# Kernel tuning notes

Hardware: AMD Instinct MI355X
Metric: run time of the kernel (lower is better)

Reference implementation:

```python
import jax, jax.numpy as jnp
import numpy as np

N, E, B = 524288, 4194304, 16384
F_IN, FP, TV, GOUT = 14, 1024, 256, 32
EPS = 1e-5
SLOPE = 0.2  # PyG GATConv default negative_slope


def setup_inputs() -> dict:
    key = jax.random.key(0)
    ks = iter(jax.random.split(key, 64))
    def nrm(shape, scale=1.0):
        return jax.random.normal(next(ks), shape, dtype=jnp.float32) * scale
    def uni(shape, lo, hi):
        return jax.random.uniform(next(ks), shape, dtype=jnp.float32, minval=lo, maxval=hi)
    def bn(d):  # [gamma, beta, running_mean, running_var]
        return jnp.stack([uni((d,), 0.5, 1.5), nrm((d,), 0.1), nrm((d,), 0.1), uni((d,), 0.5, 1.5)])
    return {
        'x': nrm((N, F_IN)),
        'edge_index': jax.random.randint(next(ks), (2, E), 0, N, dtype=jnp.int32),
        'batch': jnp.sort(jax.random.randint(next(ks), (N,), 0, B, dtype=jnp.int32)),
        'fingerprint': nrm((B, FP)),
        'transformer_features': nrm((B, TV)),
        'W1': nrm((F_IN, F_IN), 0.3), 'a_src1': nrm((F_IN,), 0.3), 'a_dst1': nrm((F_IN,), 0.3), 'b1': nrm((F_IN,), 0.1),
        'W2': nrm((F_IN, GOUT), 0.3), 'a_src2': nrm((GOUT,), 0.3), 'a_dst2': nrm((GOUT,), 0.3), 'b2': nrm((GOUT,), 0.1),
        'fc1_w': nrm((FP, 400), 0.04), 'fc1_b': nrm((400,), 0.1), 'bn1': bn(400),
        'fc2_w': nrm((400, 200), 0.07), 'fc2_b': nrm((200,), 0.1), 'bn2': bn(200),
        'fc3_w': nrm((TV, 400), 0.08), 'fc3_b': nrm((400,), 0.1), 'bn3': bn(400),
        'fc4_w': nrm((400, 200), 0.07), 'fc4_b': nrm((200,), 0.1), 'bn4': bn(200),
        'fcc1_w': nrm((GOUT + 400, 100), 0.07), 'fcc1_b': nrm((100,), 0.1), 'bnc': bn(100),
        'fcc2_w': nrm((100, 1), 0.1), 'fcc2_b': nrm((1,), 0.1),
    }


def _bn(h, p):  # eval-mode BatchNorm1d with packed params [4, d]
    return (h - p[2]) * jax.lax.rsqrt(p[3] + EPS) * p[0] + p[1]


def _gat(x, W, a_s, a_d, b, src, dst, n):
    # PyG GATConv, heads=1: messages flow src -> dst, softmax over incoming edges per dst
    h = x @ W                                   # [n, C]
    e = jax.nn.leaky_relu((h @ a_s)[src] + (h @ a_d)[dst], SLOPE)  # [E_tot]
    m = jax.lax.stop_gradient(jax.ops.segment_max(e, dst, num_segments=n))
    w = jnp.exp(e - m[dst])
    denom = jax.ops.segment_sum(w, dst, num_segments=n)
    alpha = w / denom[dst]
    out = jax.ops.segment_sum(alpha[:, None] * h[src], dst, num_segments=n)
    return out + b


def reference(x, edge_index, batch, fingerprint, transformer_features,
              W1, a_src1, a_dst1, b1, W2, a_src2, a_dst2, b2,
              fc1_w, fc1_b, bn1, fc2_w, fc2_b, bn2,
              fc3_w, fc3_b, bn3, fc4_w, fc4_b, bn4,
              fcc1_w, fcc1_b, bnc, fcc2_w, fcc2_b):
    n = x.shape[0]
    loop = jnp.arange(n, dtype=edge_index.dtype)  # add_self_loops
    src = jnp.concatenate([edge_index[0], loop])
    dst = jnp.concatenate([edge_index[1], loop])
    g = jax.nn.relu(_gat(x, W1, a_src1, a_dst1, b1, src, dst, n))
    g = jax.nn.relu(_gat(g, W2, a_src2, a_dst2, b2, src, dst, n))
    pool = jax.ops.segment_sum(g, batch, num_segments=B)  # global_add_pool -> [B, GOUT]
    fp = jax.nn.relu(_bn(fingerprint @ fc1_w + fc1_b, bn1))
    fp = jax.nn.relu(_bn(fp @ fc2_w + fc2_b, bn2))
    tv = jax.nn.relu(_bn(transformer_features @ fc3_w + fc3_b, bn3))
    tv = jax.nn.relu(_bn(tv @ fc4_w + fc4_b, bn4))
    comb = jnp.concatenate([pool, fp, tv], axis=1)  # [B, 32+200+200]
    comb = jax.nn.relu(_bn(comb @ fcc1_w + fcc1_b, bnc))
    return comb @ fcc2_w + fcc2_b  # [B, 1]
```

## Files before the change

### kernel.cpp

```cpp
#include <hip/hip_runtime.h>

typedef unsigned short u16;
typedef unsigned int u32;
typedef __attribute__((ext_vector_type(8))) short bf16x8;
typedef __attribute__((ext_vector_type(4))) float f32x4;

#define N_NODES 524288
#define N_EDGES 4194304
#define N_GRAPH 16384
#define P_BLOCKS 1024
#define BKTS 512
#define DPB 1024
#define CAP 8960

__device__ __forceinline__ float bf2f(u16 u){ u32 x=((u32)u)<<16; float f; __builtin_memcpy(&f,&x,4); return f; }
__device__ __forceinline__ float lo2f(u32 u){ u32 x=u<<16; float f; __builtin_memcpy(&f,&x,4); return f; }
__device__ __forceinline__ float hi2f(u32 u){ u32 x=u&0xffff0000u; float f; __builtin_memcpy(&f,&x,4); return f; }
__device__ __forceinline__ u16 f2bf(float f){ u32 x; __builtin_memcpy(&x,&f,4); return (u16)((x + 0x7fffu + ((x>>16)&1u))>>16); }
__device__ __forceinline__ float lrelu(float e){ return e>0.f? e : 0.2f*e; }
__device__ __forceinline__ float gload(const void* p, int i, int is32){
    return is32 ? ((const float*)p)[i] : bf2f(((const u16*)p)[i]);
}
__device__ __forceinline__ u32 fmax_key(float f){ u32 u; __builtin_memcpy(&u,&f,4); return (u>>31)? ~u : (u|0x80000000u); }
__device__ __forceinline__ float key_fmax(u32 k){ u32 u = (k>>31)? (k^0x80000000u) : ~k; float f; __builtin_memcpy(&f,&u,4); return f; }

__global__ __launch_bounds__(256) void k_detect(const u32* __restrict__ x, int* __restrict__ flag){
    __shared__ int cnt;
    if (threadIdx.x==0) cnt = 0;
    __syncthreads();
    int c = 0;
    for (int i = threadIdx.x; i < 1024; i += 256){
        u32 e = (x[i] >> 7) & 0xFF;
        if (e >= 110 && e <= 140) c++;
    }
    atomicAdd(&cnt, c);
    __syncthreads();
    if (threadIdx.x==0) *flag = (cnt < 512) ? 1 : 0;
}

__global__ __launch_bounds__(256) void k_p1(const int* __restrict__ dst, u32* __restrict__ tbl_bm){
    __shared__ u32 lh[BKTS];
    int t = threadIdx.x, blk = blockIdx.x;
    lh[t] = 0; lh[t+256] = 0;
    __syncthreads();
    int base = blk*4096;
    #pragma unroll
    for (int k=0;k<16;k++){
        int d = __builtin_nontemporal_load(dst + base + k*256 + t) & (N_NODES-1);
        atomicAdd(&lh[d>>10], 1);
    }
    __syncthreads();
    tbl_bm[blk*BKTS + t]       = lh[t];
    tbl_bm[blk*BKTS + t + 256] = lh[t+256];
}

__global__ __launch_bounds__(256) void k_ttbl(const u32* __restrict__ bm, u32* __restrict__ km){
    __shared__ u32 tile[32][33];
    int bx = blockIdx.x;
    int by = blockIdx.y;
    int tx = threadIdx.x & 31, ty = threadIdx.x >> 5;
    #pragma unroll
    for (int r=0;r<32;r+=8)
        tile[ty+r][tx] = bm[(bx*32 + ty + r)*BKTS + by*32 + tx];
    __syncthreads();
    #pragma unroll
    for (int r=0;r<32;r+=8)
        km[(by*32 + ty + r)*P_BLOCKS + bx*32 + tx] = tile[tx][ty+r];
}

__global__ __launch_bounds__(256) void k_scan1(int* __restrict__ data, int* __restrict__ bsums){
    __shared__ int sh[256];
    int b = blockIdx.x, t = threadIdx.x;
    int base = b*1024 + t*4;
    int4 v = *(const int4*)(data + base);
    int s = v.x+v.y+v.z+v.w;
    sh[t] = s; __syncthreads();
    for (int off=1; off<256; off<<=1){
        int xv = (t>=off)? sh[t-off] : 0; __syncthreads();
        sh[t] += xv; __syncthreads();
    }
    int excl = sh[t] - s;
    if (t==255) bsums[b] = sh[255];
    int4 o; o.x = excl; o.y = excl+v.x; o.z = o.y+v.y; o.w = o.z+v.z;
    *(int4*)(data + base) = o;
}

__global__ __launch_bounds__(256) void k_scan2(int* __restrict__ bsums){
    __shared__ int sh[256];
    int t = threadIdx.x;
    int v0 = bsums[2*t], v1 = bsums[2*t+1];
    int s = v0+v1; sh[t] = s; __syncthreads();
    for (int off=1; off<256; off<<=1){
        int xv = (t>=off)? sh[t-off] : 0; __syncthreads();
        sh[t] += xv; __syncthreads();
    }
    int excl = sh[t] - s;
    bsums[2*t] = excl; bsums[2*t+1] = excl + v0;
}

__global__ __launch_bounds__(256) void k_scan3(int* __restrict__ scan, const int* __restrict__ bsums, int N_, int E_){
    int i = blockIdx.x*256 + threadIdx.x;
    if (i < N_) scan[i] += bsums[i>>10];
    if (i == 0) scan[N_] = E_;
}

__global__ __launch_bounds__(256) void k_p2(const int* __restrict__ src, const int* __restrict__ dst,
        const u32* __restrict__ km, u32* __restrict__ btab){
    __shared__ u32 lh[BKTS], lofs[BKTS], gofs[BKTS];
    __shared__ u32 stage[4096], tgt[4096];
    __shared__ u32 red[256];
    int t = threadIdx.x, blk = blockIdx.x;
    lh[t] = 0; lh[t+256] = 0;
    __syncthreads();
    u32 pr[16], rk[16]; u16 bk[16];
    int base = blk*4096;
    #pragma unroll
    for (int k=0;k<16;k++){
        int e = base + k*256 + t;
        int d = __builtin_nontemporal_load(dst+e) & (N_NODES-1);
        int s = __builtin_nontemporal_load(src+e) & (N_NODES-1);
        u32 b = (u32)d >> 10;
        bk[k] = (u16)b;
        pr[k] = (u32)(d & 1023) | ((u32)s << 10);
        rk[k] = atomicAdd(&lh[b], 1);
    }
    gofs[t]       = km[(size_t)t*P_BLOCKS + blk];
    gofs[t+256]   = km[(size_t)(t+256)*P_BLOCKS + blk];
    __syncthreads();
    u32 v0 = lh[2*t], v1 = lh[2*t+1];
    u32 s2 = v0+v1; red[t] = s2; __syncthreads();
    for (int off=1; off<256; off<<=1){
        u32 xv = (t>=off)? red[t-off] : 0; __syncthreads();
        red[t] += xv; __syncthreads();
    }
    u32 excl = red[t] - s2;
    lofs[2*t] = excl; lofs[2*t+1] = excl + v0;
    __syncthreads();
    #pragma unroll
    for (int k=0;k<16;k++){
        u32 p = lofs[bk[k]] + rk[k];
        stage[p] = pr[k];
        tgt[p]   = gofs[bk[k]] + rk[k];
    }
    __syncthreads();
    #pragma unroll
    for (int k=0;k<16;k++){
        int j = k*256 + t;
        btab[tgt[j]] = stage[j];
    }
}

__global__ __launch_bounds__(256) void k_p3(const u32* __restrict__ km, const u32* __restrict__ btab,
        int* __restrict__ rowptr, int* __restrict__ ssrc){
    __shared__ u32 fh[DPB], fo[DPB];
    __shared__ u32 red[256];
    __shared__ int sst[CAP];
    int t = threadIdx.x, b = blockIdx.x;
    u32 basep = km[(size_t)b*P_BLOCKS];
    u32 endp  = km[(size_t)(b+1)*P_BLOCKS];
    int cnt = (int)(endp - basep);
    #pragma unroll
    for (int i=t;i<DPB;i+=256) fh[i] = 0;
    __syncthreads();
    for (int j=t; j<cnt; j+=256){
        u32 p = btab[basep + j];
        atomicAdd(&fh[p & 1023], 1);
    }
    __syncthreads();
    u32 v0=fh[4*t], v1=fh[4*t+1], v2=fh[4*t+2], v3=fh[4*t+3];
    u32 s4 = v0+v1+v2+v3; red[t] = s4; __syncthreads();
    for (int off=1; off<256; off<<=1){
        u32 xv = (t>=off)? red[t-off] : 0; __syncthreads();
        red[t] += xv; __syncthreads();
    }
    u32 excl = red[t] - s4;
    fo[4*t]=excl; fo[4*t+1]=excl+v0; fo[4*t+2]=excl+v0+v1; fo[4*t+3]=excl+v0+v1+v2;
    __syncthreads();
    #pragma unroll
    for (int i=t;i<DPB;i+=256) rowptr[b*DPB + i] = (int)(basep + fo[i]);
    if (b == BKTS-1 && t == 0) rowptr[N_NODES] = (int)endp;
    __syncthreads();
    for (int j=t; j<cnt; j+=256){
        u32 p = btab[basep + j];
        u32 pos = atomicAdd(&fo[p & 1023], 1);
        if (pos < (u32)CAP) sst[pos] = (int)(p >> 10);
    }
    __syncthreads();
    for (int j=t; j<cnt; j+=256) ssrc[basep + j] = sst[j];
}

__global__ __launch_bounds__(256) void k_linear1(const void* __restrict__ x,
        const void* __restrict__ W1, const void* __restrict__ asw, const void* __restrict__ adw,
        u16* __restrict__ h1, float* __restrict__ ad1, u32* __restrict__ gkey,
        const int* __restrict__ flag){
    int is32 = *flag;
    __shared__ float Wf[196], av[14], dv[14];
    __shared__ float red[256];
    int t = threadIdx.x;
    if (t < 196) Wf[t] = gload(W1, t, is32);
    else if (t < 210) av[t-196] = gload(asw, t-196, is32);
    else if (t < 224) dv[t-210] = gload(adw, t-210, is32);
    __syncthreads();
    int i = blockIdx.x*256 + t;
    float xv[14];
    if (is32){
        const float* xr = (const float*)x + (size_t)i*14;
        #pragma unroll
        for (int k=0;k<14;k++) xv[k] = xr[k];
    } else {
        const u32* xr = (const u32*)((const u16*)x + (size_t)i*14);
        #pragma unroll
        for (int p=0;p<7;p++){ u32 u = xr[p]; xv[2*p]=lo2f(u); xv[2*p+1]=hi2f(u); }
    }
    float h[14];
    #pragma unroll
    for (int j=0;j<14;j++){ float s=0.f;
        #pragma unroll
        for (int k=0;k<14;k++) s += xv[k]*Wf[k*14+j];
        h[j]=s; }
    float a=0.f, d=0.f;
    #pragma unroll
    for (int j=0;j<14;j++){ a += h[j]*av[j]; d += h[j]*dv[j]; }
    ad1[i]=d;
    u32 ou[8];
    #pragma unroll
    for (int p=0;p<7;p++) ou[p] = (u32)f2bf(h[2*p]) | ((u32)f2bf(h[2*p+1])<<16);
    __builtin_memcpy(&ou[7], &a, 4);
    uint4* hp = (uint4*)(h1 + (size_t)i*16);
    hp[0] = make_uint4(ou[0],ou[1],ou[2],ou[3]);
    hp[1] = make_uint4(ou[4],ou[5],ou[6],ou[7]);
    red[t] = a; __syncthreads();
    for (int o=128;o;o>>=1){ if (t<o) red[t]=fmaxf(red[t],red[t+o]); __syncthreads(); }
    if (t==0) atomicMax(gkey, fmax_key(red[0]));
}

__global__ __launch_bounds__(256) void k_linear2(const u16* __restrict__ g1,
        const void* __restrict__ W2, const void* __restrict__ asw, const void* __restrict__ adw,
        u16* __restrict__ h2, float* __restrict__ as2, float* __restrict__ ad2,
        u32* __restrict__ gkey, const int* __restrict__ flag){
    int is32 = *flag;
    __shared__ float Wf[448], av[32], dv[32];
    __shared__ float red[256];
    int t = threadIdx.x;
    for (int idx=t; idx<448; idx+=256) Wf[idx] = gload(W2, idx, is32);
    if (t < 32) { av[t] = gload(asw, t, is32); dv[t] = gload(adw, t, is32); }
    __syncthreads();
    int i = blockIdx.x*256 + t;
    const uint4* gp = (const uint4*)(g1 + (size_t)i*16);
    uint4 q0 = gp[0], q1 = gp[1];
    u32 u[8] = {q0.x,q0.y,q0.z,q0.w,q1.x,q1.y,q1.z,q1.w};
    float gv[14];
    #pragma unroll
    for (int k=0;k<14;k++){ u32 uu=u[k>>1]; gv[k] = (k&1)? hi2f(uu) : lo2f(uu); }
    float h[32];
    #pragma unroll
    for (int j=0;j<32;j++) h[j]=0.f;
    #pragma unroll
    for (int k=0;k<14;k++){ float g_ = gv[k];
        #pragma unroll
        for (int j=0;j<32;j++) h[j] += g_*Wf[k*32+j]; }
    float a=0.f, d=0.f;
    #pragma unroll
    for (int j=0;j<32;j++){ a += h[j]*av[j]; d += h[j]*dv[j]; }
    as2[i]=a; ad2[i]=d;
    u32 ou[16];
    #pragma unroll
    for (int p=0;p<16;p++) ou[p] = (u32)f2bf(h[2*p]) | ((u32)f2bf(h[2*p+1])<<16);
    uint4* hp = (uint4*)(h2 + (size_t)i*32);
    hp[0]=make_uint4(ou[0],ou[1],ou[2],ou[3]);
    hp[1]=make_uint4(ou[4],ou[5],ou[6],ou[7]);
    hp[2]=make_uint4(ou[8],ou[9],ou[10],ou[11]);
    hp[3]=make_uint4(ou[12],ou[13],ou[14],ou[15]);
    red[t] = a; __syncthreads();
    for (int o=128;o;o>>=1){ if (t<o) red[t]=fmaxf(red[t],red[t+o]); __syncthreads(); }
    if (t==0) atomicMax(gkey, fmax_key(red[0]));
}

__global__ __launch_bounds__(256) void k_gather1(const int* __restrict__ rowptr, const int* __restrict__ ssrc,
        const u16* __restrict__ h1, const float* __restrict__ ad1, const u32* __restrict__ gkey,
        const void* __restrict__ b1, u16* __restrict__ g1, const int* __restrict__ flag){
    int is32 = *flag;
    int i = blockIdx.x*256 + threadIdx.x;
    float adv = ad1[i];
    float M = lrelu(key_fmax(*gkey) + adv);
    int beg = rowptr[i], end = rowptr[i+1];
    float acc[14], den;
    {
        const uint4* hp = (const uint4*)(h1 + (size_t)i*16);
        uint4 q0=hp[0], q1=hp[1];
        float as_; __builtin_memcpy(&as_, &q1.w, 4);
        float w = __expf(lrelu(as_ + adv) - M); den = w;
        u32 u[7] = {q0.x,q0.y,q0.z,q0.w,q1.x,q1.y,q1.z};
        #pragma unroll
        for (int f=0;f<14;f++){ u32 uu=u[f>>1]; acc[f] = w*((f&1)? hi2f(uu):lo2f(uu)); }
    }
    for (int j=beg; j<end; j++){
        int s = __builtin_nontemporal_load(ssrc+j);
        const uint4* hp = (const uint4*)(h1 + (size_t)s*16);
        uint4 q0=hp[0], q1=hp[1];
        float as_; __builtin_memcpy(&as_, &q1.w, 4);
        float w = __expf(lrelu(as_ + adv) - M); den += w;
        u32 u[7] = {q0.x,q0.y,q0.z,q0.w,q1.x,q1.y,q1.z};
        #pragma unroll
        for (int f=0;f<14;f++){ u32 uu=u[f>>1]; acc[f] += w*((f&1)? hi2f(uu):lo2f(uu)); }
    }
    float inv = 1.0f/den;
    u32 ou[8];
    #pragma unroll
    for (int p=0;p<7;p++){
        float v0 = fmaxf(acc[2*p]*inv + gload(b1,2*p,is32), 0.f);
        float v1 = fmaxf(acc[2*p+1]*inv + gload(b1,2*p+1,is32), 0.f);
        ou[p] = (u32)f2bf(v0) | ((u32)f2bf(v1)<<16);
    }
    ou[7]=0u;
    uint4* gp = (uint4*)(g1 + (size_t)i*16);
    gp[0]=make_uint4(ou[0],ou[1],ou[2],ou[3]);
    gp[1]=make_uint4(ou[4],ou[5],ou[6],ou[7]);
}

__global__ __launch_bounds__(256) void k_gather2(const int* __restrict__ rowptr, const int* __restrict__ ssrc,
        const u16* __restrict__ h2, const float* __restrict__ as2, const float* __restrict__ ad2,
        const u32* __restrict__ gkey, const void* __restrict__ b2, u16* __restrict__ g2,
        const int* __restrict__ flag){
    int is32 = *flag;
    int i = blockIdx.x*256 + threadIdx.x;
    float adv = ad2[i];
    float M = lrelu(key_fmax(*gkey) + adv);
    int beg = rowptr[i], end = rowptr[i+1];
    float acc[32], den;
    {
        float w = __expf(lrelu(as2[i] + adv) - M); den = w;
        const uint4* hp = (const uint4*)(h2 + (size_t)i*32);
        uint4 q0=hp[0], q1=hp[1], q2=hp[2], q3=hp[3];
        u32 u[16] = {q0.x,q0.y,q0.z,q0.w,q1.x,q1.y,q1.z,q1.w,q2.x,q2.y,q2.z,q2.w,q3.x,q3.y,q3.z,q3.w};
        #pragma unroll
        for (int f=0;f<32;f++){ u32 uu=u[f>>1]; acc[f] = w*((f&1)? hi2f(uu):lo2f(uu)); }
    }
    for (int j=beg; j<end; j++){
        int s = __builtin_nontemporal_load(ssrc+j);
        float w = __expf(lrelu(as2[s] + adv) - M); den += w;
        const uint4* hp = (const uint4*)(h2 + (size_t)s*32);
        uint4 q0=hp[0], q1=hp[1], q2=hp[2], q3=hp[3];
        u32 u[16] = {q0.x,q0.y,q0.z,q0.w,q1.x,q1.y,q1.z,q1.w,q2.x,q2.y,q2.z,q2.w,q3.x,q3.y,q3.z,q3.w};
        #pragma unroll
        for (int f=0;f<32;f++){ u32 uu=u[f>>1]; acc[f] += w*((f&1)? hi2f(uu):lo2f(uu)); }
    }
    float inv = 1.0f/den;
    u32 ou[16];
    #pragma unroll
    for (int p=0;p<16;p++){
        float v0 = fmaxf(acc[2*p]*inv + gload(b2,2*p,is32), 0.f);
        float v1 = fmaxf(acc[2*p+1]*inv + gload(b2,2*p+1,is32), 0.f);
        ou[p] = (u32)f2bf(v0) | ((u32)f2bf(v1)<<16);
    }
    uint4* gp = (uint4*)(g2 + (size_t)i*32);
    gp[0]=make_uint4(ou[0],ou[1],ou[2],ou[3]);
    gp[1]=make_uint4(ou[4],ou[5],ou[6],ou[7]);
    gp[2]=make_uint4(ou[8],ou[9],ou[10],ou[11]);
    gp[3]=make_uint4(ou[12],ou[13],ou[14],ou[15]);
}

__device__ __forceinline__ int lbound(const int* __restrict__ a, int n, int v){
    int lo=0, hi=n;
    while (lo < hi){ int m = (lo+hi)>>1; if (a[m] < v) lo = m+1; else hi = m; }
    return lo;
}

__global__ __launch_bounds__(64) void k_pool(const u16* __restrict__ g2, const int* __restrict__ batch,
        u16* __restrict__ comb, int N_){
    int b = blockIdx.x;
    int t = threadIdx.x, f = t & 31, half = t >> 5;
    int lo = lbound(batch, N_, b);
    int hi = lbound(batch, N_, b+1);
    float acc = 0.f;
    for (int i = lo + half; i < hi; i += 2) acc += bf2f(g2[(size_t)i*32 + f]);
    acc += __shfl_xor(acc, 32);
    if (t < 32) comb[(size_t)b*432 + f] = f2bf(acc);
}

__global__ __launch_bounds__(256) void k_transpose(const void* __restrict__ W, u16* __restrict__ Wt,
        int K, int Kp, int Nc, const int* __restrict__ flag){
    int is32 = *flag;
    int idx = blockIdx.x*256 + threadIdx.x;
    if (idx >= Nc*Kp) return;
    int n = idx / Kp, k = idx - n*Kp;
    Wt[idx] = (k < K) ? f2bf(gload(W, k*Nc + n, is32)) : (u16)0;
}

__global__ __launch_bounds__(256) void k_gemm(const void* __restrict__ A, const u16* __restrict__ Wt,
        const void* __restrict__ bias, const void* __restrict__ bnp, void* __restrict__ out,
        int K, int Kp, int Nc, int ostride, int ooff, int do_relu,
        int afollow, int out32, const int* __restrict__ flag){
    int is32 = *flag;
    int a32 = afollow ? is32 : 0;
    __shared__ u16 As[128][40];
    __shared__ u16 Bs[128][40];
    int t = threadIdx.x;
    int lane = t & 63, wave = t >> 6;
    int bm = blockIdx.x * 128;
    int bn = blockIdx.y * 128;
    int mt = (wave & 1) * 64, nt = (wave >> 1) * 64;
    int quad = lane >> 4, fr = lane & 15;

    f32x4 zero = {0.f, 0.f, 0.f, 0.f};
    f32x4 acc[4][4];
    #pragma unroll
    for (int i=0;i<4;i++)
        #pragma unroll
        for (int j=0;j<4;j++) acc[i][j] = zero;

    int srow0 = t >> 2;
    int scol = (t & 3) * 8;

    for (int k0 = 0; k0 < Kp; k0 += 32){
        #pragma unroll
        for (int h2_=0; h2_<2; h2_++){
            int row = srow0 + h2_*64;
            int gk = k0 + scol;
            if (a32){
                float4 a0 = {0,0,0,0}, a1 = {0,0,0,0};
                if (gk + 8 <= K){
                    const float* ap = (const float*)A + (size_t)(bm+row)*K + gk;
                    a0 = *(const float4*)ap; a1 = *(const float4*)(ap+4);
                }
                u32 w0 = (u32)f2bf(a0.x) | ((u32)f2bf(a0.y)<<16);
                u32 w1 = (u32)f2bf(a0.z) | ((u32)f2bf(a0.w)<<16);
                u32 w2 = (u32)f2bf(a1.x) | ((u32)f2bf(a1.y)<<16);
                u32 w3 = (u32)f2bf(a1.z) | ((u32)f2bf(a1.w)<<16);
                *(uint4*)(&As[row][scol]) = make_uint4(w0,w1,w2,w3);
            } else {
                uint4 av = make_uint4(0,0,0,0);
                if (gk + 8 <= K) av = *(const uint4*)((const u16*)A + (size_t)(bm+row)*K + gk);
                *(uint4*)(&As[row][scol]) = av;
            }
            uint4 bv = make_uint4(0,0,0,0);
            if (bn + row < Nc) bv = *(const uint4*)(Wt + (size_t)(bn+row)*Kp + gk);
            *(uint4*)(&Bs[row][scol]) = bv;
        }
        __syncthreads();
        bf16x8 af[4], bfr[4];
        #pragma unroll
        for (int i=0;i<4;i++) af[i] = *(const bf16x8*)(&As[mt + i*16 + fr][quad*8]);
        #pragma unroll
        for (int j=0;j<4;j++) bfr[j] = *(const bf16x8*)(&Bs[nt + j*16 + fr][quad*8]);
        #pragma unroll
        for (int i=0;i<4;i++)
            #pragma unroll
            for (int j=0;j<4;j++)
                acc[i][j] = __builtin_amdgcn_mfma_f32_16x16x32_bf16(af[i], bfr[j], acc[i][j], 0, 0, 0);
        __syncthreads();
    }

    #pragma unroll
    for (int j=0;j<4;j++){
        int gn = bn + nt + j*16 + fr;
        if (gn >= Nc) continue;
        float bb = gload(bias, gn, is32);
        float scale = 1.f, shift = bb;
        if (bnp){
            float gm_ = gload(bnp, gn, is32), bt = gload(bnp, Nc+gn, is32);
            float mn = gload(bnp, 2*Nc+gn, is32), vr = gload(bnp, 3*Nc+gn, is32);
            scale = gm_ * rsqrtf(vr + 1e-5f);
            shift = (bb - mn)*scale + bt;
        }
        #pragma unroll
        for (int i=0;i<4;i++){
            #pragma unroll
            for (int r=0;r<4;r++){
                int gm = bm + mt + i*16 + quad*4 + r;
                float v = acc[i][j][r]*scale + shift;
                if (do_relu) v = fmaxf(v, 0.f);
                size_t oidx = (size_t)gm*ostride + ooff + gn;
                if (out32) ((float*)out)[oidx] = v;
                else       ((u16*)out)[oidx] = f2bf(v);
            }
        }
    }
}

__global__ __launch_bounds__(256) void k_fcc2(const float* __restrict__ c1, const void* __restrict__ w,
        const void* __restrict__ b, float* __restrict__ outp, const int* __restrict__ flag){
    int is32 = *flag;
    __shared__ float wf[100];
    int t = threadIdx.x;
    if (t < 100) wf[t] = gload(w, t, is32);
    __syncthreads();
    int i = blockIdx.x*256 + t;
    const float* r = c1 + (size_t)i*100;
    float s = 0.f;
    #pragma unroll 4
    for (int k=0;k<100;k++) s += r[k]*wf[k];
    outp[i] = s + gload(b, 0, is32);
}

extern "C" void kernel_launch(void* const* d_in, const int* in_sizes, int n_in,
                              void* d_out, int out_size, void* d_ws, size_t ws_size,
                              hipStream_t stream){
    const int N = N_NODES, E = N_EDGES;
    const void* x    = d_in[0];
    const int* ei   = (const int*)d_in[1];
    const int* srcA = ei;
    const int* dstA = ei + E;
    const int* batch= (const int*)d_in[2];
    const void* fing = d_in[3];
    const void* tv   = d_in[4];
    const void* W1   = d_in[5];
    const void* as1w = d_in[6];
    const void* ad1w = d_in[7];
    const void* b1   = d_in[8];
    const void* W2   = d_in[9];
    const void* as2w = d_in[10];
    const void* ad2w = d_in[11];
    const void* b2   = d_in[12];
    const void* fc1w = d_in[13]; const void* fc1b = d_in[14]; const void* bn1 = d_in[15];
    const void* fc2w = d_in[16]; const void* fc2b = d_in[17]; const void* bn2 = d_in[18];
    const void* fc3w = d_in[19]; const void* fc3b = d_in[20]; const void* bn3 = d_in[21];
    const void* fc4w = d_in[22]; const void* fc4b = d_in[23]; const void* bn4 = d_in[24];
    const void* fccw = d_in[25]; const void* fccb = d_in[26]; const void* bnc = d_in[27];
    const void* fcc2w= d_in[28]; const void* fcc2b= d_in[29];

    char* ws = (char*)d_ws;
    size_t off = 0;
    auto alloc = [&](size_t bytes)->char*{ char* p = ws + off; off = (off + bytes + 255) & ~(size_t)255; return p; };
    int*  flagp  = (int*)alloc(256);
    u32*  gkey1  = (u32*)flagp + 1;
    u32*  gkey2  = (u32*)flagp + 2;
    int*  rowptr = (int*)alloc((size_t)(N+1)*4);
    int*  bsums  = (int*)alloc(513*4);
    u32*  tbl_bm = (u32*)alloc((size_t)BKTS*P_BLOCKS*4);
    u32*  tbl_km = (u32*)alloc(((size_t)BKTS*P_BLOCKS+1)*4);
    int*  ssrc   = (int*)alloc((size_t)E*4);
    u16*  h1     = (u16*)alloc((size_t)N*16*2);
    u16*  g1     = (u16*)alloc((size_t)N*16*2);
    float* ad1_  = (float*)alloc((size_t)N*4);
    float* as2_  = (float*)alloc((size_t)N*4);
    float* ad2_  = (float*)alloc((size_t)N*4);
    u16*  h2     = (u16*)alloc((size_t)N*32*2);
    float* c1    = (float*)alloc((size_t)N_GRAPH*100*4);
    u16*  Wt1    = (u16*)alloc((size_t)400*1024*2);
    u16*  Wt2    = (u16*)alloc((size_t)200*416*2);
    u16*  Wt3    = (u16*)alloc((size_t)400*256*2);
    u16*  Wt4    = (u16*)alloc((size_t)200*416*2);
    u16*  Wtc    = (u16*)alloc((size_t)100*448*2);
    u16*  g2     = h1;
    u16*  comb   = (u16*)ssrc;
    u32*  btab   = (u32*)h2;
    u16*  fp1    = h2;
    u16*  tv1    = h2 + (size_t)N_GRAPH*400;

    (void)hipMemsetAsync(flagp, 0, 256, stream);

    k_detect <<<1, 256, 0, stream>>>((const u32*)x, flagp);

    k_p1   <<<P_BLOCKS, 256, 0, stream>>>(dstA, tbl_bm);
    k_ttbl <<<dim3(32,16), 256, 0, stream>>>(tbl_bm, tbl_km);
    k_scan1<<<512,  256, 0, stream>>>((int*)tbl_km, bsums);
    k_scan2<<<1,    256, 0, stream>>>(bsums);
    k_scan3<<<(BKTS*P_BLOCKS)/256, 256, 0, stream>>>((int*)tbl_km, bsums, BKTS*P_BLOCKS, E);
    k_p2   <<<P_BLOCKS, 256, 0, stream>>>(srcA, dstA, tbl_km, btab);
    k_p3   <<<BKTS, 256, 0, stream>>>(tbl_km, btab, rowptr, ssrc);

    k_linear1<<<N/256, 256, 0, stream>>>(x, W1, as1w, ad1w, h1, ad1_, gkey1, flagp);
    k_gather1<<<N/256, 256, 0, stream>>>(rowptr, ssrc, h1, ad1_, gkey1, b1, g1, flagp);
    k_linear2<<<N/256, 256, 0, stream>>>(g1, W2, as2w, ad2w, h2, as2_, ad2_, gkey2, flagp);
    k_gather2<<<N/256, 256, 0, stream>>>(rowptr, ssrc, h2, as2_, ad2_, gkey2, b2, g2, flagp);
    k_pool   <<<N_GRAPH, 64, 0, stream>>>(g2, batch, comb, N);

    k_transpose<<<(400*1024+255)/256, 256, 0, stream>>>(fc1w, Wt1, 1024, 1024, 400, flagp);
    k_transpose<<<(200*416 +255)/256, 256, 0, stream>>>(fc2w, Wt2,  400,  416, 200, flagp);
    k_transpose<<<(400*256 +255)/256, 256, 0, stream>>>(fc3w, Wt3,  256,  256, 400, flagp);
    k_transpose<<<(200*416 +255)/256, 256, 0, stream>>>(fc4w, Wt4,  400,  416, 200, flagp);
    k_transpose<<<(100*448 +255)/256, 256, 0, stream>>>(fccw, Wtc,  432,  448, 100, flagp);

    k_gemm<<<dim3(128,4), 256, 0, stream>>>(fing, Wt1, fc1b, bn1, fp1, 1024, 1024, 400, 400,   0, 1, 1, 0, flagp);
    k_gemm<<<dim3(128,2), 256, 0, stream>>>(fp1,  Wt2, fc2b, bn2, comb, 400,  416, 200, 432,  32, 1, 0, 0, flagp);
    k_gemm<<<dim3(128,4), 256, 0, stream>>>(tv,   Wt3, fc3b, bn3, tv1,  256,  256, 400, 400,   0, 1, 1, 0, flagp);
    k_gemm<<<dim3(128,2), 256, 0, stream>>>(tv1,  Wt4, fc4b, bn4, comb, 400,  416, 200, 432, 232, 1, 0, 0, flagp);
    k_gemm<<<dim3(128,1), 256, 0, stream>>>(comb, Wtc, fccb, bnc, c1,   432,  448, 100, 100,   0, 1, 0, 1, flagp);

    k_fcc2<<<N_GRAPH/256, 256, 0, stream>>>(c1, fcc2w, fcc2b, (float*)d_out, flagp);
}
```

Measured before the change: 780.7 us.

## Aggregate GAT layer 2 in 14-dim input space and apply W2 after aggregation

Layer 2 now aggregates the 14-wide layer-1 outputs and multiplies by W2 after the softmax-weighted sum, which is valid because aggregation is linear. The separate linear2 kernel goes away, and the per-edge gather shrinks from 64-byte to 32-byte rows. The attention projections are folded into W2 @ a_src/a_dst vectors by a tiny prep kernel and computed inside gather1, which also writes the layer-2 max key. The gather loops are unrolled by four to keep more loads in flight, and fp32 inputs are pre-cast to bf16 by a separate kernel so the GEMM drops its fp32 path; this adds some extra kernels and traffic for the casts.

```diff
diff --git a/kernel.cpp b/kernel.cpp
--- a/kernel.cpp
+++ b/kernel.cpp
@@ -24,6 +24,15 @@
 __device__ __forceinline__ u32 fmax_key(float f){ u32 u; __builtin_memcpy(&u,&f,4); return (u>>31)? ~u : (u|0x80000000u); }
 __device__ __forceinline__ float key_fmax(u32 k){ u32 u = (k>>31)? (k^0x80000000u) : ~k; float f; __builtin_memcpy(&f,&u,4); return f; }
 
+__device__ __forceinline__ void edge_acc(uint4 q0, uint4 q1, float adv, float M,
+        float* acc, float& den){
+    float as_; __builtin_memcpy(&as_, &q1.w, 4);
+    float w = __expf(lrelu(as_ + adv) - M); den += w;
+    u32 u[7] = {q0.x,q0.y,q0.z,q0.w,q1.x,q1.y,q1.z};
+    #pragma unroll
+    for (int f=0;f<14;f++){ u32 uu=u[f>>1]; acc[f] += w*((f&1)? hi2f(uu):lo2f(uu)); }
+}
+
 __global__ __launch_bounds__(256) void k_detect(const u32* __restrict__ x, int* __restrict__ flag){
     __shared__ int cnt;
     if (threadIdx.x==0) cnt = 0;
@@ -38,6 +47,38 @@
     if (threadIdx.x==0) *flag = (cnt < 512) ? 1 : 0;
 }
 
+__global__ __launch_bounds__(64) void k_prep(const void* __restrict__ W2, const void* __restrict__ asw,
+        const void* __restrict__ adw, float* __restrict__ prep, const int* __restrict__ flag){
+    int is32 = *flag;
+    int t = threadIdx.x;
+    if (t < 28){
+        int j = t % 14, which = t / 14;
+        const void* av = which ? adw : asw;
+        float s = 0.f;
+        #pragma unroll
+        for (int k=0;k<32;k++) s += gload(W2, j*32+k, is32) * gload(av, k, is32);
+        prep[which*14 + j] = s;
+    }
+}
+
+__global__ __launch_bounds__(256) void k_cast(const void* __restrict__ in, u16* __restrict__ out,
+        int n8, const int* __restrict__ flag){
+    int is32 = *flag;
+    int idx = blockIdx.x*256 + threadIdx.x;
+    if (idx >= n8) return;
+    if (is32){
+        const float4* ip = (const float4*)in + idx*2;
+        float4 a0 = ip[0], a1 = ip[1];
+        u32 w0 = (u32)f2bf(a0.x) | ((u32)f2bf(a0.y)<<16);
+        u32 w1 = (u32)f2bf(a0.z) | ((u32)f2bf(a0.w)<<16);
+        u32 w2 = (u32)f2bf(a1.x) | ((u32)f2bf(a1.y)<<16);
+        u32 w3 = (u32)f2bf(a1.z) | ((u32)f2bf(a1.w)<<16);
+        ((uint4*)out)[idx] = make_uint4(w0,w1,w2,w3);
+    } else {
+        ((uint4*)out)[idx] = ((const uint4*)in)[idx];
+    }
+}
+
 __global__ __launch_bounds__(256) void k_p1(const int* __restrict__ dst, u32* __restrict__ tbl_bm){
     __shared__ u32 lh[BKTS];
     int t = threadIdx.x, blk = blockIdx.x;
@@ -56,8 +97,7 @@
 
 __global__ __launch_bounds__(256) void k_ttbl(const u32* __restrict__ bm, u32* __restrict__ km){
     __shared__ u32 tile[32][33];
-    int bx = blockIdx.x;
-    int by = blockIdx.y;
+    int bx = blockIdx.x, by = blockIdx.y;
     int tx = threadIdx.x & 31, ty = threadIdx.x >> 5;
     #pragma unroll
     for (int r=0;r<32;r+=8)
@@ -234,130 +274,126 @@
     if (t==0) atomicMax(gkey, fmax_key(red[0]));
 }
 
-__global__ __launch_bounds__(256) void k_linear2(const u16* __restrict__ g1,
-        const void* __restrict__ W2, const void* __restrict__ asw, const void* __restrict__ adw,
-        u16* __restrict__ h2, float* __restrict__ as2, float* __restrict__ ad2,
-        u32* __restrict__ gkey, const int* __restrict__ flag){
-    int is32 = *flag;
-    __shared__ float Wf[448], av[32], dv[32];
+__global__ __launch_bounds__(256) void k_gather1(const int* __restrict__ rowptr, const int* __restrict__ ssrc,
+        const u16* __restrict__ h1, const float* __restrict__ ad1, const u32* __restrict__ gkey1,
+        const void* __restrict__ b1, const float* __restrict__ prep,
+        u16* __restrict__ g1, float* __restrict__ ad2, u32* __restrict__ gkey2,
+        const int* __restrict__ flag){
+    int is32 = *flag;
+    __shared__ float b1s[14], vas[14], vds[14];
     __shared__ float red[256];
     int t = threadIdx.x;
-    for (int idx=t; idx<448; idx+=256) Wf[idx] = gload(W2, idx, is32);
-    if (t < 32) { av[t] = gload(asw, t, is32); dv[t] = gload(adw, t, is32); }
+    if (t < 14) b1s[t] = gload(b1, t, is32);
+    else if (t < 28) vas[t-14] = prep[t-14];
+    else if (t < 42) vds[t-28] = prep[t-28+14];
     __syncthreads();
     int i = blockIdx.x*256 + t;
-    const uint4* gp = (const uint4*)(g1 + (size_t)i*16);
-    uint4 q0 = gp[0], q1 = gp[1];
-    u32 u[8] = {q0.x,q0.y,q0.z,q0.w,q1.x,q1.y,q1.z,q1.w};
-    float gv[14];
-    #pragma unroll
-    for (int k=0;k<14;k++){ u32 uu=u[k>>1]; gv[k] = (k&1)? hi2f(uu) : lo2f(uu); }
-    float h[32];
-    #pragma unroll
-    for (int j=0;j<32;j++) h[j]=0.f;
-    #pragma unroll
-    for (int k=0;k<14;k++){ float g_ = gv[k];
-        #pragma unroll
-        for (int j=0;j<32;j++) h[j] += g_*Wf[k*32+j]; }
-    float a=0.f, d=0.f;
-    #pragma unroll
-    for (int j=0;j<32;j++){ a += h[j]*av[j]; d += h[j]*dv[j]; }
-    as2[i]=a; ad2[i]=d;
-    u32 ou[16];
-    #pragma unroll
-    for (int p=0;p<16;p++) ou[p] = (u32)f2bf(h[2*p]) | ((u32)f2bf(h[2*p+1])<<16);
-    uint4* hp = (uint4*)(h2 + (size_t)i*32);
-    hp[0]=make_uint4(ou[0],ou[1],ou[2],ou[3]);
-    hp[1]=make_uint4(ou[4],ou[5],ou[6],ou[7]);
-    hp[2]=make_uint4(ou[8],ou[9],ou[10],ou[11]);
-    hp[3]=make_uint4(ou[12],ou[13],ou[14],ou[15]);
-    red[t] = a; __syncthreads();
-    for (int o=128;o;o>>=1){ if (t<o) red[t]=fmaxf(red[t],red[t+o]); __syncthreads(); }
-    if (t==0) atomicMax(gkey, fmax_key(red[0]));
-}
-
-__global__ __launch_bounds__(256) void k_gather1(const int* __restrict__ rowptr, const int* __restrict__ ssrc,
-        const u16* __restrict__ h1, const float* __restrict__ ad1, const u32* __restrict__ gkey,
-        const void* __restrict__ b1, u16* __restrict__ g1, const int* __restrict__ flag){
-    int is32 = *flag;
-    int i = blockIdx.x*256 + threadIdx.x;
     float adv = ad1[i];
-    float M = lrelu(key_fmax(*gkey) + adv);
+    float M = lrelu(key_fmax(*gkey1) + adv);
     int beg = rowptr[i], end = rowptr[i+1];
-    float acc[14], den;
+    float acc[14] = {0,0,0,0,0,0,0,0,0,0,0,0,0,0};
+    float den = 0.f;
     {
         const uint4* hp = (const uint4*)(h1 + (size_t)i*16);
-        uint4 q0=hp[0], q1=hp[1];
-        float as_; __builtin_memcpy(&as_, &q1.w, 4);
-        float w = __expf(lrelu(as_ + adv) - M); den = w;
-        u32 u[7] = {q0.x,q0.y,q0.z,q0.w,q1.x,q1.y,q1.z};
-        #pragma unroll
-        for (int f=0;f<14;f++){ u32 uu=u[f>>1]; acc[f] = w*((f&1)? hi2f(uu):lo2f(uu)); }
-    }
-    for (int j=beg; j<end; j++){
-        int s = __builtin_nontemporal_load(ssrc+j);
+        edge_acc(hp[0], hp[1], adv, M, acc, den);
+    }
+    int j = beg;
+    for (; j+4 <= end; j += 4){
+        int s4[4];
+        #pragma unroll
+        for (int k=0;k<4;k++) s4[k] = __builtin_nontemporal_load(ssrc + j + k);
+        uint4 r0[4], r1[4];
+        #pragma unroll
+        for (int k=0;k<4;k++){
+            const uint4* hp = (const uint4*)(h1 + (size_t)s4[k]*16);
+            r0[k] = hp[0]; r1[k] = hp[1];
+        }
+        #pragma unroll
+        for (int k=0;k<4;k++) edge_acc(r0[k], r1[k], adv, M, acc, den);
+    }
+    for (; j<end; j++){
+        int s = __builtin_nontemporal_load(ssrc + j);
         const uint4* hp = (const uint4*)(h1 + (size_t)s*16);
-        uint4 q0=hp[0], q1=hp[1];
-        float as_; __builtin_memcpy(&as_, &q1.w, 4);
-        float w = __expf(lrelu(as_ + adv) - M); den += w;
-        u32 u[7] = {q0.x,q0.y,q0.z,q0.w,q1.x,q1.y,q1.z};
-        #pragma unroll
-        for (int f=0;f<14;f++){ u32 uu=u[f>>1]; acc[f] += w*((f&1)? hi2f(uu):lo2f(uu)); }
+        edge_acc(hp[0], hp[1], adv, M, acc, den);
     }
     float inv = 1.0f/den;
+    float v[14];
+    #pragma unroll
+    for (int f=0;f<14;f++) v[f] = fmaxf(acc[f]*inv + b1s[f], 0.f);
+    float a2=0.f, d2=0.f;
+    #pragma unroll
+    for (int f=0;f<14;f++){ a2 += v[f]*vas[f]; d2 += v[f]*vds[f]; }
+    ad2[i] = d2;
     u32 ou[8];
     #pragma unroll
-    for (int p=0;p<7;p++){
-        float v0 = fmaxf(acc[2*p]*inv + gload(b1,2*p,is32), 0.f);
-        float v1 = fmaxf(acc[2*p+1]*inv + gload(b1,2*p+1,is32), 0.f);
-        ou[p] = (u32)f2bf(v0) | ((u32)f2bf(v1)<<16);
-    }
-    ou[7]=0u;
+    for (int p=0;p<7;p++) ou[p] = (u32)f2bf(v[2*p]) | ((u32)f2bf(v[2*p+1])<<16);
+    __builtin_memcpy(&ou[7], &a2, 4);
     uint4* gp = (uint4*)(g1 + (size_t)i*16);
     gp[0]=make_uint4(ou[0],ou[1],ou[2],ou[3]);
     gp[1]=make_uint4(ou[4],ou[5],ou[6],ou[7]);
+    red[t] = a2; __syncthreads();
+    for (int o=128;o;o>>=1){ if (t<o) red[t]=fmaxf(red[t],red[t+o]); __syncthreads(); }
+    if (t==0) atomicMax(gkey2, fmax_key(red[0]));
 }
 
 __global__ __launch_bounds__(256) void k_gather2(const int* __restrict__ rowptr, const int* __restrict__ ssrc,
-        const u16* __restrict__ h2, const float* __restrict__ as2, const float* __restrict__ ad2,
-        const u32* __restrict__ gkey, const void* __restrict__ b2, u16* __restrict__ g2,
+        const u16* __restrict__ g1, const float* __restrict__ ad2, const u32* __restrict__ gkey2,
+        const void* __restrict__ W2, const void* __restrict__ b2, u16* __restrict__ g2,
         const int* __restrict__ flag){
     int is32 = *flag;
-    int i = blockIdx.x*256 + threadIdx.x;
+    __shared__ float W2s[448], b2s[32];
+    int t = threadIdx.x;
+    for (int idx=t; idx<448; idx+=256) W2s[idx] = gload(W2, idx, is32);
+    if (t < 32) b2s[t] = gload(b2, t, is32);
+    __syncthreads();
+    int i = blockIdx.x*256 + t;
     float adv = ad2[i];
-    float M = lrelu(key_fmax(*gkey) + adv);
+    float M = lrelu(key_fmax(*gkey2) + adv);
     int beg = rowptr[i], end = rowptr[i+1];
-    float acc[32], den;
+    float acc[14] = {0,0,0,0,0,0,0,0,0,0,0,0,0,0};
+    float den = 0.f;
     {
-        float w = __expf(lrelu(as2[i] + adv) - M); den = w;
-        const uint4* hp = (const uint4*)(h2 + (size_t)i*32);
-        uint4 q0=hp[0], q1=hp[1], q2=hp[2], q3=hp[3];
-        u32 u[16] = {q0.x,q0.y,q0.z,q0.w,q1.x,q1.y,q1.z,q1.w,q2.x,q2.y,q2.z,q2.w,q3.x,q3.y,q3.z,q3.w};
-        #pragma unroll
-        for (int f=0;f<32;f++){ u32 uu=u[f>>1]; acc[f] = w*((f&1)? hi2f(uu):lo2f(uu)); }
-    }
-    for (int j=beg; j<end; j++){
-        int s = __builtin_nontemporal_load(ssrc+j);
-        float w = __expf(lrelu(as2[s] + adv) - M); den += w;
-        const uint4* hp = (const uint4*)(h2 + (size_t)s*32);
-        uint4 q0=hp[0], q1=hp[1], q2=hp[2], q3=hp[3];
-        u32 u[16] = {q0.x,q0.y,q0.z,q0.w,q1.x,q1.y,q1.z,q1.w,q2.x,q2.y,q2.z,q2.w,q3.x,q3.y,q3.z,q3.w};
-        #pragma unroll
-        for (int f=0;f<32;f++){ u32 uu=u[f>>1]; acc[f] += w*((f&1)? hi2f(uu):lo2f(uu)); }
+        const uint4* hp = (const uint4*)(g1 + (size_t)i*16);
+        edge_acc(hp[0], hp[1], adv, M, acc, den);
+    }
+    int j = beg;
+    for (; j+4 <= end; j += 4){
+        int s4[4];
+        #pragma unroll
+        for (int k=0;k<4;k++) s4[k] = __builtin_nontemporal_load(ssrc + j + k);
+        uint4 r0[4], r1[4];
+        #pragma unroll
+        for (int k=0;k<4;k++){
+            const uint4* hp = (const uint4*)(g1 + (size_t)s4[k]*16);
+            r0[k] = hp[0]; r1[k] = hp[1];
+        }
+        #pragma unroll
+        for (int k=0;k<4;k++) edge_acc(r0[k], r1[k], adv, M, acc, den);
+    }
+    for (; j<end; j++){
+        int s = __builtin_nontemporal_load(ssrc + j);
+        const uint4* hp = (const uint4*)(g1 + (size_t)s*16);
+        edge_acc(hp[0], hp[1], adv, M, acc, den);
     }
     float inv = 1.0f/den;
-    u32 ou[16];
-    #pragma unroll
-    for (int p=0;p<16;p++){
-        float v0 = fmaxf(acc[2*p]*inv + gload(b2,2*p,is32), 0.f);
-        float v1 = fmaxf(acc[2*p+1]*inv + gload(b2,2*p+1,is32), 0.f);
-        ou[p] = (u32)f2bf(v0) | ((u32)f2bf(v1)<<16);
-    }
-    uint4* gp = (uint4*)(g2 + (size_t)i*32);
-    gp[0]=make_uint4(ou[0],ou[1],ou[2],ou[3]);
-    gp[1]=make_uint4(ou[4],ou[5],ou[6],ou[7]);
-    gp[2]=make_uint4(ou[8],ou[9],ou[10],ou[11]);
-    gp[3]=make_uint4(ou[12],ou[13],ou[14],ou[15]);
+    float an[14];
+    #pragma unroll
+    for (int f=0;f<14;f++) an[f] = acc[f]*inv;
+    uint4* orow = (uint4*)(g2 + (size_t)i*32);
+    #pragma unroll
+    for (int g=0; g<4; g++){
+        u32 ou[4];
+        #pragma unroll
+        for (int p=0;p<4;p++){
+            int j0 = g*8 + 2*p;
+            float va_ = b2s[j0], vb_ = b2s[j0+1];
+            #pragma unroll
+            for (int k=0;k<14;k++){ va_ += an[k]*W2s[k*32+j0]; vb_ += an[k]*W2s[k*32+j0+1]; }
+            va_ = fmaxf(va_, 0.f); vb_ = fmaxf(vb_, 0.f);
+            ou[p] = (u32)f2bf(va_) | ((u32)f2bf(vb_)<<16);
+        }
+        orow[g] = make_uint4(ou[0],ou[1],ou[2],ou[3]);
+    }
 }
 
 __device__ __forceinline__ int lbound(const int* __restrict__ a, int n, int v){
@@ -390,9 +426,8 @@
 __global__ __launch_bounds__(256) void k_gemm(const void* __restrict__ A, const u16* __restrict__ Wt,
         const void* __restrict__ bias, const void* __restrict__ bnp, void* __restrict__ out,
         int K, int Kp, int Nc, int ostride, int ooff, int do_relu,
-        int afollow, int out32, const int* __restrict__ flag){
-    int is32 = *flag;
-    int a32 = afollow ? is32 : 0;
+        int out32, const int* __restrict__ flag){
+    int is32 = *flag;
     __shared__ u16 As[128][40];
     __shared__ u16 Bs[128][40];
     int t = threadIdx.x;
@@ -417,22 +452,9 @@
         for (int h2_=0; h2_<2; h2_++){
             int row = srow0 + h2_*64;
             int gk = k0 + scol;
-            if (a32){
-                float4 a0 = {0,0,0,0}, a1 = {0,0,0,0};
-                if (gk + 8 <= K){
-                    const float* ap = (const float*)A + (size_t)(bm+row)*K + gk;
-                    a0 = *(const float4*)ap; a1 = *(const float4*)(ap+4);
-                }
-                u32 w0 = (u32)f2bf(a0.x) | ((u32)f2bf(a0.y)<<16);
-                u32 w1 = (u32)f2bf(a0.z) | ((u32)f2bf(a0.w)<<16);
-                u32 w2 = (u32)f2bf(a1.x) | ((u32)f2bf(a1.y)<<16);
-                u32 w3 = (u32)f2bf(a1.z) | ((u32)f2bf(a1.w)<<16);
-                *(uint4*)(&As[row][scol]) = make_uint4(w0,w1,w2,w3);
-            } else {
-                uint4 av = make_uint4(0,0,0,0);
-                if (gk + 8 <= K) av = *(const uint4*)((const u16*)A + (size_t)(bm+row)*K + gk);
-                *(uint4*)(&As[row][scol]) = av;
-            }
+            uint4 av = make_uint4(0,0,0,0);
+            if (gk + 8 <= K) av = *(const uint4*)((const u16*)A + (size_t)(bm+row)*K + gk);
+            *(uint4*)(&As[row][scol]) = av;
             uint4 bv = make_uint4(0,0,0,0);
             if (bn + row < Nc) bv = *(const uint4*)(Wt + (size_t)(bn+row)*Kp + gk);
             *(uint4*)(&Bs[row][scol]) = bv;
@@ -525,6 +547,7 @@
     int*  flagp  = (int*)alloc(256);
     u32*  gkey1  = (u32*)flagp + 1;
     u32*  gkey2  = (u32*)flagp + 2;
+    float* prep  = (float*)((char*)flagp + 16);
     int*  rowptr = (int*)alloc((size_t)(N+1)*4);
     int*  bsums  = (int*)alloc(513*4);
     u32*  tbl_bm = (u32*)alloc((size_t)BKTS*P_BLOCKS*4);
@@ -533,24 +556,27 @@
     u16*  h1     = (u16*)alloc((size_t)N*16*2);
     u16*  g1     = (u16*)alloc((size_t)N*16*2);
     float* ad1_  = (float*)alloc((size_t)N*4);
-    float* as2_  = (float*)alloc((size_t)N*4);
     float* ad2_  = (float*)alloc((size_t)N*4);
-    u16*  h2     = (u16*)alloc((size_t)N*32*2);
+    char* scr32  = alloc((size_t)N*32*2);
     float* c1    = (float*)alloc((size_t)N_GRAPH*100*4);
     u16*  Wt1    = (u16*)alloc((size_t)400*1024*2);
     u16*  Wt2    = (u16*)alloc((size_t)200*416*2);
     u16*  Wt3    = (u16*)alloc((size_t)400*256*2);
     u16*  Wt4    = (u16*)alloc((size_t)200*416*2);
     u16*  Wtc    = (u16*)alloc((size_t)100*448*2);
-    u16*  g2     = h1;
+    u16*  tv_bf  = (u16*)alloc((size_t)N_GRAPH*256*2);
+    u32*  btab   = (u32*)scr32;
+    u16*  g2     = (u16*)scr32;
+    u16*  fp1    = (u16*)scr32;
+    u16*  tv1    = (u16*)scr32 + (size_t)N_GRAPH*400;
     u16*  comb   = (u16*)ssrc;
-    u32*  btab   = (u32*)h2;
-    u16*  fp1    = h2;
-    u16*  tv1    = h2 + (size_t)N_GRAPH*400;
+    u16*  fing_bf= h1;
 
     (void)hipMemsetAsync(flagp, 0, 256, stream);
 
     k_detect <<<1, 256, 0, stream>>>((const u32*)x, flagp);
+    k_prep   <<<1, 64, 0, stream>>>(W2, as2w, ad2w, prep, flagp);
+    k_cast   <<<(N_GRAPH*256/8+255)/256, 256, 0, stream>>>(tv, tv_bf, N_GRAPH*256/8, flagp);
 
     k_p1   <<<P_BLOCKS, 256, 0, stream>>>(dstA, tbl_bm);
     k_ttbl <<<dim3(32,16), 256, 0, stream>>>(tbl_bm, tbl_km);
@@ -561,9 +587,9 @@
     k_p3   <<<BKTS, 256, 0, stream>>>(tbl_km, btab, rowptr, ssrc);
 
     k_linear1<<<N/256, 256, 0, stream>>>(x, W1, as1w, ad1w, h1, ad1_, gkey1, flagp);
-    k_gather1<<<N/256, 256, 0, stream>>>(rowptr, ssrc, h1, ad1_, gkey1, b1, g1, flagp);
-    k_linear2<<<N/256, 256, 0, stream>>>(g1, W2, as2w, ad2w, h2, as2_, ad2_, gkey2, flagp);
-    k_gather2<<<N/256, 256, 0, stream>>>(rowptr, ssrc, h2, as2_, ad2_, gkey2, b2, g2, flagp);
+    k_gather1<<<N/256, 256, 0, stream>>>(rowptr, ssrc, h1, ad1_, gkey1, b1, prep, g1, ad2_, gkey2, flagp);
+    k_gather2<<<N/256, 256, 0, stream>>>(rowptr, ssrc, g1, ad2_, gkey2, W2, b2, g2, flagp);
+    k_cast   <<<(N_GRAPH*1024/8+255)/256, 256, 0, stream>>>(fing, fing_bf, N_GRAPH*1024/8, flagp);
     k_pool   <<<N_GRAPH, 64, 0, stream>>>(g2, batch, comb, N);
 
     k_transpose<<<(400*1024+255)/256, 256, 0, stream>>>(fc1w, Wt1, 1024, 1024, 400, flagp);
@@ -572,11 +598,11 @@
     k_transpose<<<(200*416 +255)/256, 256, 0, stream>>>(fc4w, Wt4,  400,  416, 200, flagp);
     k_transpose<<<(100*448 +255)/256, 256, 0, stream>>>(fccw, Wtc,  432,  448, 100, flagp);
 
-    k_gemm<<<dim3(128,4), 256, 0, stream>>>(fing, Wt1, fc1b, bn1, fp1, 1024, 1024, 400, 400,   0, 1, 1, 0, flagp);
-    k_gemm<<<dim3(128,2), 256, 0, stream>>>(fp1,  Wt2, fc2b, bn2, comb, 400,  416, 200, 432,  32, 1, 0, 0, flagp);
-    k_gemm<<<dim3(128,4), 256, 0, stream>>>(tv,   Wt3, fc3b, bn3, tv1,  256,  256, 400, 400,   0, 1, 1, 0, flagp);
-    k_gemm<<<dim3(128,2), 256, 0, stream>>>(tv1,  Wt4, fc4b, bn4, comb, 400,  416, 200, 432, 232, 1, 0, 0, flagp);
-    k_gemm<<<dim3(128,1), 256, 0, stream>>>(comb, Wtc, fccb, bnc, c1,   432,  448, 100, 100,   0, 1, 0, 1, flagp);
+    k_gemm<<<dim3(128,4), 256, 0, stream>>>(fing_bf, Wt1, fc1b, bn1, fp1, 1024, 1024, 400, 400,   0, 1, 0, flagp);
+    k_gemm<<<dim3(128,2), 256, 0, stream>>>(fp1,  Wt2, fc2b, bn2, comb, 400,  416, 200, 432,  32, 1, 0, flagp);
+    k_gemm<<<dim3(128,4), 256, 0, stream>>>(tv_bf, Wt3, fc3b, bn3, tv1, 256,  256, 400, 400,   0, 1, 0, flagp);
+    k_gemm<<<dim3(128,2), 256, 0, stream>>>(tv1,  Wt4, fc4b, bn4, comb, 400,  416, 200, 432, 232, 1, 0, flagp);
+    k_gemm<<<dim3(128,1), 256, 0, stream>>>(comb, Wtc, fccb, bnc, c1,   432,  448, 100, 100,   0, 1, 1, flagp);
 
     k_fcc2<<<N_GRAPH/256, 256, 0, stream>>>(c1, fcc2w, fcc2b, (float*)d_out, flagp);
 }
```

After: 730.0 us. -6.5%, faster.
